# Kernel optimization log

Hardware: AMD Instinct MI355X
Metric: run time of the kernel (lower is better)

The kernel has to match this reference:

```python
import jax, jax.numpy as jnp
import numpy as np

B, T, C, H = 4, 2048, 1024, 16


def setup_inputs() -> dict:
    key = jax.random.key(0)
    k1, k2, k3 = jax.random.split(key, 3)
    x = jax.random.normal(k1, (B, T, C), dtype=jnp.float32)
    Wqkv = jax.random.normal(k2, (C, 3 * C), dtype=jnp.float32) * 0.02
    bqkv = jnp.zeros((3 * C,), dtype=jnp.float32)
    Wproj = jax.random.normal(k3, (C, C), dtype=jnp.float32) * 0.02
    bproj = jnp.zeros((C,), dtype=jnp.float32)
    return {"x": x, "Wqkv": Wqkv, "bqkv": bqkv, "Wproj": Wproj, "bproj": bproj}


def reference(x, Wqkv, bqkv, Wproj, bproj):
    Bx, Tx, Cx = x.shape
    head = Cx // H
    qkv = x @ Wqkv + bqkv                      # [B,T,3C]
    q, k, v = jnp.split(qkv, 3, axis=-1)
    q = q.reshape(Bx, Tx, H, head)
    k = k.reshape(Bx, Tx, H, head)
    v = v.reshape(Bx, Tx, H, head)
    scale = 1.0 / jnp.sqrt(jnp.asarray(head, dtype=x.dtype))
    scores = jnp.einsum('bqhd,bkhd->bhqk', q, k) * scale   # [B,H,T,T]
    causal = jnp.tril(jnp.ones((Tx, Tx), dtype=bool))       # [T,T]
    neg = jnp.finfo(x.dtype).min
    scores = jnp.where(causal[None, None, :, :], scores, neg)
    probs = jax.nn.softmax(scores, axis=-1)
    y = jnp.einsum('bhqk,bkhd->bqhd', probs, v).reshape(Bx, Tx, Cx)
    return y @ Wproj + bproj
```

## Files before the change

### kernel.cpp

```cpp
#include <hip/hip_runtime.h>
#include <stdint.h>

#define BB 4
#define TT 2048
#define CC 1024
#define HH 16

typedef __bf16 bf16x8 __attribute__((ext_vector_type(8)));
typedef float f32x4 __attribute__((ext_vector_type(4)));
typedef float f32x16 __attribute__((ext_vector_type(16)));
typedef unsigned short ushort8 __attribute__((ext_vector_type(8)));
typedef unsigned short ushort4v __attribute__((ext_vector_type(4)));

__device__ __forceinline__ unsigned short f2b(float f) {
    union { float f; unsigned u; } v; v.f = f;
    unsigned r = v.u + 0x7FFFu + ((v.u >> 16) & 1u);
    return (unsigned short)(r >> 16);
}
__device__ __forceinline__ unsigned pack2(float a, float b) {
    union { float f; unsigned u; } ua, ub; ua.f = a; ub.f = b;
    return __builtin_amdgcn_perm(ub.u + 0x8000u, ua.u + 0x8000u, 0x07060302u);
}
__device__ __forceinline__ float fexp2(float x) {
#if __has_builtin(__builtin_amdgcn_exp2f)
    return __builtin_amdgcn_exp2f(x);
#else
    return exp2f(x);
#endif
}
#define LOG2E 1.4426950408889634f

#define ASYNC16(gp, lp) __builtin_amdgcn_global_load_lds( \
    (const __attribute__((address_space(1))) void*)(gp),  \
    (__attribute__((address_space(3))) void*)(lp), 16, 0, 0)

__global__ __launch_bounds__(256) void k_cast(const float* __restrict__ in,
                                              unsigned short* __restrict__ out, int n) {
    int i = (blockIdx.x * 256 + threadIdx.x) * 4;
    if (i >= n) return;
    float4 v = *(const float4*)(in + i);
    ushort4v o;
    o.x = f2b(v.x); o.y = f2b(v.y); o.z = f2b(v.z); o.w = f2b(v.w);
    *(ushort4v*)(out + i) = o;
}

__global__ __launch_bounds__(256) void k_transpose_bf16(const float* __restrict__ in,
                                                        unsigned short* __restrict__ out,
                                                        int R, int Cc) {
    __shared__ float tile[32][33];
    int bx = blockIdx.x * 32, by = blockIdx.y * 32;
    int tx = threadIdx.x, ty = threadIdx.y;
    for (int i = 0; i < 32; i += 8)
        tile[ty + i][tx] = in[(size_t)(by + ty + i) * Cc + bx + tx];
    __syncthreads();
    for (int i = 0; i < 32; i += 8)
        out[(size_t)(bx + ty + i) * R + by + tx] = f2b(tile[tx][ty + i]);
}

#define QSCALE 0.125f
template <int MODE>
__global__ __launch_bounds__(256) void k_gemm(const unsigned short* __restrict__ A,
                                              const unsigned short* __restrict__ Bt,
                                              const float* __restrict__ bias,
                                              float* __restrict__ outf,
                                              unsigned short* __restrict__ qo,
                                              unsigned short* __restrict__ ko,
                                              unsigned short* __restrict__ vo,
                                              int M, int N, int K) {
    __shared__ unsigned short As[128 * 32];
    __shared__ unsigned short Bs[128 * 32];
    const int t = threadIdx.x;
    const int lane = t & 63;
    const int c = lane & 15, qd = lane >> 4;
    const int wave = t >> 6;
    const int wr = (wave >> 1) * 64, wc = (wave & 1) * 64;
    const int bm = blockIdx.x * 128, bn = blockIdx.y * 128;

    f32x4 acc[4][4] = {};

    const unsigned short* Ap = A + (size_t)(bm + (t >> 2)) * K + (t & 3) * 8;
    const unsigned short* Bp = Bt + (size_t)(bn + (t >> 2)) * K + (t & 3) * 8;
    unsigned short* Asw = &As[t * 8];
    unsigned short* Bsw = &Bs[t * 8];

    for (int k0 = 0; k0 < K; k0 += 32) {
        __syncthreads();
        ASYNC16(Ap + k0, Asw);
        ASYNC16(Ap + (size_t)64 * K + k0, Asw + 2048);
        ASYNC16(Bp + k0, Bsw);
        ASYNC16(Bp + (size_t)64 * K + k0, Bsw + 2048);
        __syncthreads();
        bf16x8 af[4], bfr[4];
        for (int i = 0; i < 4; i++)
            af[i] = *(const bf16x8*)&As[(wr + i * 16 + c) * 32 + qd * 8];
        for (int j = 0; j < 4; j++)
            bfr[j] = *(const bf16x8*)&Bs[(wc + j * 16 + c) * 32 + qd * 8];
        for (int i = 0; i < 4; i++)
            for (int j = 0; j < 4; j++)
                acc[i][j] = __builtin_amdgcn_mfma_f32_16x16x32_bf16(af[i], bfr[j], acc[i][j], 0, 0, 0);
    }

    if (MODE == 0) {
        for (int i = 0; i < 4; i++) {
            int row0 = bm + wr + i * 16 + qd * 4;
            for (int j = 0; j < 4; j++) {
                int col = bn + wc + j * 16 + c;
                float bv = bias[col];
                for (int r = 0; r < 4; r++)
                    outf[(size_t)(row0 + r) * N + col] = acc[i][j][r] + bv;
            }
        }
    } else {
        if (bn < 1024) {
            for (int i = 0; i < 4; i++) {
                int row0 = bm + wr + i * 16 + qd * 4;
                for (int j = 0; j < 4; j++) {
                    int col = bn + wc + j * 16 + c;
                    float bv = bias[col];
                    for (int r = 0; r < 4; r++)
                        qo[(size_t)(row0 + r) * 1024 + col] = f2b((acc[i][j][r] + bv) * QSCALE);
                }
            }
        } else if (bn < 2048) {
            for (int i = 0; i < 4; i++) {
                int row0 = bm + wr + i * 16 + qd * 4;
                for (int j = 0; j < 4; j++) {
                    int col = bn + wc + j * 16 + c;
                    float bv = bias[col];
                    for (int r = 0; r < 4; r++)
                        ko[(size_t)(row0 + r) * 1024 + (col - 1024)] = f2b(acc[i][j][r] + bv);
                }
            }
        } else {
            int b = bm >> 11;
            int tb = (bm & 2047) + wr;
            for (int i = 0; i < 4; i++) {
                int t0 = tb + i * 16 + qd * 4;
                for (int j = 0; j < 4; j++) {
                    int col = bn + wc + j * 16 + c;
                    float bv = bias[col];
                    int d = col - 2048;
                    int hh = d >> 6, dl = d & 63;
                    ushort4v pk;
                    pk.x = f2b(acc[i][j][0] + bv); pk.y = f2b(acc[i][j][1] + bv);
                    pk.z = f2b(acc[i][j][2] + bv); pk.w = f2b(acc[i][j][3] + bv);
                    *(ushort4v*)&vo[(((size_t)b * 16 + hh) * 64 + dl) * TT + t0] = pk;
                }
            }
        }
    }
}

__global__ __launch_bounds__(256, 4) void k_attn(const unsigned short* __restrict__ q16,
                                                 const unsigned short* __restrict__ k16,
                                                 const unsigned short* __restrict__ vT16,
                                                 unsigned short* __restrict__ y16) {
    const int h = blockIdx.y, b = blockIdx.z;
    const int qi = (((int)blockIdx.x + h) & 15) ^ ((b & 1) ? 15 : 0);
    __shared__ unsigned short q_s[128 * 72];
    __shared__ unsigned short k_s[64 * 72];
    __shared__ unsigned short vt_s[64 * 72];
    const int t = threadIdx.x, lane = t & 63, wave = t >> 6;
    const int l31 = lane & 31, hl = lane >> 5;
    const int wq = wave * 32;

    {
        int row = t >> 1, c32 = (t & 1) * 32;
        const unsigned short* src = q16 + ((size_t)(b * TT + qi * 128 + row)) * CC + h * 64 + c32;
        ushort8 v0 = *(const ushort8*)(src);
        ushort8 v1 = *(const ushort8*)(src + 8);
        ushort8 v2 = *(const ushort8*)(src + 16);
        ushort8 v3 = *(const ushort8*)(src + 24);
        *(ushort8*)&q_s[row * 72 + c32] = v0;
        *(ushort8*)&q_s[row * 72 + c32 + 8] = v1;
        *(ushort8*)&q_s[row * 72 + c32 + 16] = v2;
        *(ushort8*)&q_s[row * 72 + c32 + 24] = v3;
    }
    __syncthreads();
    bf16x8 qf[4];
    for (int s = 0; s < 4; s++)
        qf[s] = *(const bf16x8*)&q_s[(wq + l31) * 72 + s * 16 + hl * 8];

    f32x16 oacc[2] = {};
    float m = -3e38f, l = 0.f;
    const int qmaxw = qi * 128 + wq + 31;
    const int qminw = qi * 128 + wq;
    const int qg = qi * 128 + wq + l31;
    const int jn = 2 * qi + 2;
    const unsigned short* kbase = k16 + (size_t)b * TT * CC + h * 64;
    const unsigned short* vbase = vT16 + (((size_t)b * 16 + h) * 64) * TT;

    const int row = t >> 2, c16 = (t & 3) * 16;
    const unsigned short* ksrc = kbase + (size_t)row * CC + c16;
    const unsigned short* vsrc = vbase + (size_t)row * TT + c16;
    ushort8 ka = *(const ushort8*)ksrc, kb = *(const ushort8*)(ksrc + 8);
    ushort8 va = *(const ushort8*)vsrc, vb = *(const ushort8*)(vsrc + 8);

    for (int j = 0; j < jn; j++) {
        __syncthreads();
        *(ushort8*)&k_s[row * 72 + c16] = ka;
        *(ushort8*)&k_s[row * 72 + c16 + 8] = kb;
        *(ushort8*)&vt_s[row * 72 + c16] = va;
        *(ushort8*)&vt_s[row * 72 + c16 + 8] = vb;
        __syncthreads();
        if (j + 1 < jn) {
            const unsigned short* kn = ksrc + (size_t)(j + 1) * 64 * CC;
            const unsigned short* vn = vsrc + (j + 1) * 64;
            ka = *(const ushort8*)kn; kb = *(const ushort8*)(kn + 8);
            va = *(const ushort8*)vn; vb = *(const ushort8*)(vn + 8);
        }
        if (j * 64 > qmaxw) continue;

        f32x16 sacc[2] = {};
        for (int c2 = 0; c2 < 2; c2++)
            for (int s = 0; s < 4; s++) {
                bf16x8 kf = *(const bf16x8*)&k_s[(c2 * 32 + l31) * 72 + s * 16 + hl * 8];
                sacc[c2] = __builtin_amdgcn_mfma_f32_32x32x16_bf16(kf, qf[s], sacc[c2], 0, 0, 0);
            }

        if (j * 64 + 63 > qminw) {
            for (int c2 = 0; c2 < 2; c2++)
                for (int r = 0; r < 16; r++) {
                    int kvg = j * 64 + c2 * 32 + (r & 3) + 8 * (r >> 2) + 4 * hl;
                    if (kvg > qg) sacc[c2][r] = -1e30f;
                }
        }

        float mx = -1e30f;
        for (int c2 = 0; c2 < 2; c2++)
            for (int r = 0; r < 16; r++) mx = fmaxf(mx, sacc[c2][r]);
        mx = fmaxf(mx, __shfl_xor(mx, 32, 64));
        float mn = fmaxf(m, mx);
        float negmnl = -mn * LOG2E;
        float alpha = fexp2(fmaf(m, LOG2E, negmnl));
        m = mn;
        float sum = 0.f;
        unsigned pg[2][4][2];
        for (int c2 = 0; c2 < 2; c2++)
            for (int g = 0; g < 4; g++) {
                float p0 = fexp2(fmaf(sacc[c2][g * 4 + 0], LOG2E, negmnl));
                float p1 = fexp2(fmaf(sacc[c2][g * 4 + 1], LOG2E, negmnl));
                float p2 = fexp2(fmaf(sacc[c2][g * 4 + 2], LOG2E, negmnl));
                float p3 = fexp2(fmaf(sacc[c2][g * 4 + 3], LOG2E, negmnl));
                sum += (p0 + p1) + (p2 + p3);
                pg[c2][g][0] = pack2(p0, p1);
                pg[c2][g][1] = pack2(p2, p3);
            }
        sum += __shfl_xor(sum, 32, 64);
        l = l * alpha + sum;
        if (__ballot(alpha != 1.0f)) {
            for (int c2 = 0; c2 < 2; c2++)
                for (int r = 0; r < 16; r++) oacc[c2][r] *= alpha;
        }

        bf16x8 pf[4];
        for (int c2 = 0; c2 < 2; c2++)
            for (int pr = 0; pr < 2; pr++) {
                unsigned se0 = hl ? pg[c2][2 * pr][0] : pg[c2][2 * pr + 1][0];
                unsigned se1 = hl ? pg[c2][2 * pr][1] : pg[c2][2 * pr + 1][1];
                unsigned r0 = (unsigned)__shfl_xor((int)se0, 32, 64);
                unsigned r1 = (unsigned)__shfl_xor((int)se1, 32, 64);
                union { unsigned u[4]; bf16x8 v; } fr;
                fr.u[0] = hl ? r0 : pg[c2][2 * pr][0];
                fr.u[1] = hl ? r1 : pg[c2][2 * pr][1];
                fr.u[2] = hl ? pg[c2][2 * pr + 1][0] : r0;
                fr.u[3] = hl ? pg[c2][2 * pr + 1][1] : r1;
                pf[c2 * 2 + pr] = fr.v;
            }

        for (int s = 0; s < 4; s++)
            for (int c2o = 0; c2o < 2; c2o++) {
                bf16x8 vf = *(const bf16x8*)&vt_s[(c2o * 32 + l31) * 72 + s * 16 + hl * 8];
                oacc[c2o] = __builtin_amdgcn_mfma_f32_32x32x16_bf16(vf, pf[s], oacc[c2o], 0, 0, 0);
            }
    }

    float rl = 1.0f / l;
    size_t rowb = ((size_t)b * TT + qg) * CC + h * 64;
    for (int c2 = 0; c2 < 2; c2++)
        for (int g = 0; g < 4; g++) {
            ushort4v pk;
            pk.x = f2b(oacc[c2][g * 4 + 0] * rl);
            pk.y = f2b(oacc[c2][g * 4 + 1] * rl);
            pk.z = f2b(oacc[c2][g * 4 + 2] * rl);
            pk.w = f2b(oacc[c2][g * 4 + 3] * rl);
            *(ushort4v*)&y16[rowb + c2 * 32 + g * 8 + hl * 4] = pk;
        }
}

extern "C" void kernel_launch(void* const* d_in, const int* in_sizes, int n_in,
                              void* d_out, int out_size, void* d_ws, size_t ws_size,
                              hipStream_t stream) {
    const float* x     = (const float*)d_in[0];
    const float* Wqkv  = (const float*)d_in[1];
    const float* bqkv  = (const float*)d_in[2];
    const float* Wproj = (const float*)d_in[3];
    const float* bproj = (const float*)d_in[4];
    float* out = (float*)d_out;

    const int M = BB * TT;
    unsigned short* x16    = (unsigned short*)d_ws;
    unsigned short* y16    = x16;
    unsigned short* wqkvT  = x16 + (size_t)M * CC;
    unsigned short* wprojT = wqkvT + (size_t)3 * CC * CC;
    unsigned short* q16    = wprojT + (size_t)CC * CC;
    unsigned short* k16    = q16 + (size_t)M * CC;
    unsigned short* vT16   = k16 + (size_t)M * CC;

    k_cast<<<(M * CC) / 1024, 256, 0, stream>>>(x, x16, M * CC);
    k_transpose_bf16<<<dim3(3 * CC / 32, CC / 32), dim3(32, 8), 0, stream>>>(Wqkv, wqkvT, CC, 3 * CC);
    k_transpose_bf16<<<dim3(CC / 32, CC / 32), dim3(32, 8), 0, stream>>>(Wproj, wprojT, CC, CC);
    k_gemm<1><<<dim3(M / 128, 3 * CC / 128), 256, 0, stream>>>(x16, wqkvT, bqkv, nullptr,
                                                               q16, k16, vT16, M, 3 * CC, CC);
    k_attn<<<dim3(TT / 128, HH, BB), 256, 0, stream>>>(q16, k16, vT16, y16);
    k_gemm<0><<<dim3(M / 128, CC / 128), 256, 0, stream>>>(y16, wprojT, bproj, out,
                                                           nullptr, nullptr, nullptr, M, CC, CC);
}
```

Before: 281.2 us.

## Stage GEMM epilogue through LDS for coalesced stores; alias attention LDS buffers

The GEMM epilogue adds the bias once in registers, then stages each output tile through shared memory. It writes back with 16-byte row-contiguous stores, including the transposed V layout, instead of scattered 2- and 4-byte stores. The attention kernel makes the Q staging buffer share memory with the K buffer, which shrinks its LDS footprint, and raises the launch bound to 8 blocks per CU for more occupancy. The costs are extra barriers and LDS traffic in the epilogue, register pressure under the tighter launch bound, and correctness that depends on Q being fully read into registers before K overwrites it.

```diff
diff --git a/kernel.cpp b/kernel.cpp
--- a/kernel.cpp
+++ b/kernel.cpp
@@ -67,8 +67,9 @@
                                               unsigned short* __restrict__ ko,
                                               unsigned short* __restrict__ vo,
                                               int M, int N, int K) {
-    __shared__ unsigned short As[128 * 32];
-    __shared__ unsigned short Bs[128 * 32];
+    __shared__ unsigned short sm[8704];
+    unsigned short* As = sm;
+    unsigned short* Bs = sm + 4096;
     const int t = threadIdx.x;
     const int lane = t & 63;
     const int c = lane & 15, qd = lane >> 4;
@@ -100,66 +101,94 @@
                 acc[i][j] = __builtin_amdgcn_mfma_f32_16x16x32_bf16(af[i], bfr[j], acc[i][j], 0, 0, 0);
     }
 
+    for (int j = 0; j < 4; j++) {
+        float bv = bias[bn + wc + j * 16 + c];
+        for (int i = 0; i < 4; i++)
+            for (int r = 0; r < 4; r++)
+                acc[i][j][r] += bv;
+    }
+
     if (MODE == 0) {
-        for (int i = 0; i < 4; i++) {
-            int row0 = bm + wr + i * 16 + qd * 4;
+        float* smf = (float*)sm;
+        for (int p = 0; p < 4; p++) {
+            __syncthreads();
+            int lr0 = (wr >> 2) + qd * 4;
             for (int j = 0; j < 4; j++) {
-                int col = bn + wc + j * 16 + c;
-                float bv = bias[col];
+                int col = wc + j * 16 + c;
                 for (int r = 0; r < 4; r++)
-                    outf[(size_t)(row0 + r) * N + col] = acc[i][j][r] + bv;
+                    smf[(lr0 + r) * 132 + col] = acc[p][j][r];
+            }
+            __syncthreads();
+            for (int op = 0; op < 4; op++) {
+                int lr = (t >> 5) + op * 8;
+                int ch = (t & 31) * 4;
+                float4 v = *(float4*)&smf[lr * 132 + ch];
+                int grow = bm + (lr >> 4) * 64 + 16 * p + (lr & 15);
+                *(float4*)&outf[(size_t)grow * N + bn + ch] = v;
+            }
+        }
+    } else if (bn < 2048) {
+        unsigned short* dst = (bn < 1024) ? qo : ko;
+        const int dcol0 = (bn < 1024) ? bn : bn - 1024;
+        const float sc = (bn < 1024) ? QSCALE : 1.0f;
+        for (int p = 0; p < 2; p++) {
+            __syncthreads();
+            for (int ii = 0; ii < 2; ii++) {
+                int i = 2 * p + ii;
+                int lr0 = (wr >> 1) + ii * 16 + qd * 4;
+                for (int j = 0; j < 4; j++) {
+                    int col = wc + j * 16 + c;
+                    for (int r = 0; r < 4; r++)
+                        sm[(lr0 + r) * 136 + col] = f2b(acc[i][j][r] * sc);
+                }
+            }
+            __syncthreads();
+            for (int op = 0; op < 4; op++) {
+                int lr = (t >> 4) + op * 16;
+                int ch = (t & 15) * 8;
+                ushort8 v = *(ushort8*)&sm[lr * 136 + ch];
+                int grow = bm + (lr >> 5) * 64 + 32 * p + (lr & 31);
+                *(ushort8*)&dst[(size_t)grow * 1024 + dcol0 + ch] = v;
             }
         }
     } else {
-        if (bn < 1024) {
-            for (int i = 0; i < 4; i++) {
-                int row0 = bm + wr + i * 16 + qd * 4;
-                for (int j = 0; j < 4; j++) {
-                    int col = bn + wc + j * 16 + c;
-                    float bv = bias[col];
-                    for (int r = 0; r < 4; r++)
-                        qo[(size_t)(row0 + r) * 1024 + col] = f2b((acc[i][j][r] + bv) * QSCALE);
+        const int bseg = bm >> 11;
+        const int bmt = bm & 2047;
+        for (int p = 0; p < 2; p++) {
+            __syncthreads();
+            for (int jj = 0; jj < 2; jj++) {
+                int j = 2 * p + jj;
+                int dl = (wc >> 1) + jj * 16 + c;
+                for (int i = 0; i < 4; i++) {
+                    int tl = wr + i * 16 + qd * 4;
+                    ushort4v pk;
+                    pk.x = f2b(acc[i][j][0]); pk.y = f2b(acc[i][j][1]);
+                    pk.z = f2b(acc[i][j][2]); pk.w = f2b(acc[i][j][3]);
+                    *(ushort4v*)&sm[dl * 136 + tl] = pk;
                 }
             }
-        } else if (bn < 2048) {
-            for (int i = 0; i < 4; i++) {
-                int row0 = bm + wr + i * 16 + qd * 4;
-                for (int j = 0; j < 4; j++) {
-                    int col = bn + wc + j * 16 + c;
-                    float bv = bias[col];
-                    for (int r = 0; r < 4; r++)
-                        ko[(size_t)(row0 + r) * 1024 + (col - 1024)] = f2b(acc[i][j][r] + bv);
-                }
-            }
-        } else {
-            int b = bm >> 11;
-            int tb = (bm & 2047) + wr;
-            for (int i = 0; i < 4; i++) {
-                int t0 = tb + i * 16 + qd * 4;
-                for (int j = 0; j < 4; j++) {
-                    int col = bn + wc + j * 16 + c;
-                    float bv = bias[col];
-                    int d = col - 2048;
-                    int hh = d >> 6, dl = d & 63;
-                    ushort4v pk;
-                    pk.x = f2b(acc[i][j][0] + bv); pk.y = f2b(acc[i][j][1] + bv);
-                    pk.z = f2b(acc[i][j][2] + bv); pk.w = f2b(acc[i][j][3] + bv);
-                    *(ushort4v*)&vo[(((size_t)b * 16 + hh) * 64 + dl) * TT + t0] = pk;
-                }
-            }
-        }
-    }
-}
-
-__global__ __launch_bounds__(256, 4) void k_attn(const unsigned short* __restrict__ q16,
+            __syncthreads();
+            for (int op = 0; op < 4; op++) {
+                int dl = (t >> 4) + op * 16;
+                int ch = (t & 15) * 8;
+                ushort8 v = *(ushort8*)&sm[dl * 136 + ch];
+                int d = (bn - 2048) + (dl >> 5) * 64 + 32 * p + (dl & 31);
+                *(ushort8*)&vo[((size_t)bseg * 1024 + d) * 2048 + bmt + ch] = v;
+            }
+        }
+    }
+}
+
+__global__ __launch_bounds__(256, 8) void k_attn(const unsigned short* __restrict__ q16,
                                                  const unsigned short* __restrict__ k16,
                                                  const unsigned short* __restrict__ vT16,
                                                  unsigned short* __restrict__ y16) {
     const int h = blockIdx.y, b = blockIdx.z;
     const int qi = (((int)blockIdx.x + h) & 15) ^ ((b & 1) ? 15 : 0);
-    __shared__ unsigned short q_s[128 * 72];
-    __shared__ unsigned short k_s[64 * 72];
-    __shared__ unsigned short vt_s[64 * 72];
+    __shared__ unsigned short smem[128 * 72];
+    unsigned short* q_s = smem;
+    unsigned short* k_s = smem;
+    unsigned short* vt_s = smem + 64 * 72;
     const int t = threadIdx.x, lane = t & 63, wave = t >> 6;
     const int l31 = lane & 31, hl = lane >> 5;
     const int wq = wave * 32;
```

Measured after the change: 686.8 us. 2.44x slower.
